# Performance work log

Measured on AMD Instinct MI355X. Metric: run time of the kernel, lower is better.

## Reference

```python
import jax, jax.numpy as jnp
import numpy as np

B, Hh, Ww, C = 32, 56, 56, 256
WIN, SHIFT, HEADS = 7, 3, 8
N = WIN * WIN
nW = (Hh // WIN) * (Ww // WIN)


def _rel_pos_index(w):
    coords = np.stack(np.meshgrid(np.arange(w), np.arange(w), indexing='ij'))  # (2,w,w)
    flat = coords.reshape(2, -1)
    rel = (flat[:, :, None] - flat[:, None, :]).transpose(1, 2, 0)  # (N,N,2)
    rel[..., 0] += w - 1
    rel[..., 1] += w - 1
    rel[..., 0] *= 2 * w - 1
    return rel.sum(-1)  # (N,N) int


def _shift_attn_mask(H, W, w, s):
    img = np.zeros((H, W))
    cnt = 0
    for hs in (slice(0, -w), slice(-w, -s), slice(-s, None)):
        for ws in (slice(0, -w), slice(-w, -s), slice(-s, None)):
            img[hs, ws] = cnt
            cnt += 1
    mw = img.reshape(H // w, w, W // w, w).transpose(0, 2, 1, 3).reshape(-1, w * w)  # (nW,N)
    diff = mw[:, None, :] - mw[:, :, None]
    return np.where(diff != 0, -100.0, 0.0).astype(np.float32)  # (nW,N,N)


REL_IDX = jnp.asarray(_rel_pos_index(WIN))


def layer_norm(x, g, b):
    m = x.mean(-1, keepdims=True)
    v = ((x - m) ** 2).mean(-1, keepdims=True)
    return (x - m) / jnp.sqrt(v + 1e-5) * g + b


def setup_inputs() -> dict:
    key = jax.random.key(0)
    ks = jax.random.split(key, 10)
    s02 = 0.02
    x = jax.random.normal(ks[0], (B, Hh * Ww, C), jnp.float32)
    qkv_w = jax.random.normal(ks[1], (3 * C, C), jnp.float32) * s02
    qkv_b = jnp.zeros((3 * C,), jnp.float32)
    rpb_table = jax.random.normal(ks[2], ((2 * WIN - 1) ** 2, HEADS), jnp.float32) * s02
    proj_w = jax.random.normal(ks[3], (C, C), jnp.float32) * s02
    proj_b = jnp.zeros((C,), jnp.float32)
    fc1_w = jax.random.normal(ks[4], (4 * C, C), jnp.float32) * s02
    fc1_b = jnp.zeros((4 * C,), jnp.float32)
    fc2_w = jax.random.normal(ks[5], (C, 4 * C), jnp.float32) * s02
    fc2_b = jnp.zeros((C,), jnp.float32)
    attn_mask = jnp.asarray(_shift_attn_mask(Hh, Ww, WIN, SHIFT))
    # saliency masks: per-token binary fg/bg -> additive 0/-100 key masks
    fg_tok = jax.random.bernoulli(ks[6], 0.5, (B * nW, N))
    sal_fg = jnp.where(fg_tok[:, None, :], 0.0, -100.0) * jnp.ones((1, N, 1), jnp.float32)
    sal_bg = jnp.where(fg_tok[:, None, :], -100.0, 0.0) * jnp.ones((1, N, 1), jnp.float32)
    return dict(x=x, qkv_w=qkv_w, qkv_b=qkv_b, rpb_table=rpb_table, proj_w=proj_w,
                proj_b=proj_b, norm1_g=jnp.ones((C,)), norm1_b=jnp.zeros((C,)),
                norm2_g=jnp.ones((C,)), norm2_b=jnp.zeros((C,)),
                fc1_w=fc1_w, fc1_b=fc1_b, fc2_w=fc2_w, fc2_b=fc2_b,
                attn_mask=attn_mask, sal_fg_attn_mask=sal_fg.astype(jnp.float32),
                sal_bg_attn_mask=sal_bg.astype(jnp.float32))


def reference(x, qkv_w, qkv_b, rpb_table, proj_w, proj_b, norm1_g, norm1_b,
              norm2_g, norm2_b, fc1_w, fc1_b, fc2_w, fc2_b,
              attn_mask, sal_fg_attn_mask, sal_bg_attn_mask):
    Bb, L, Cc = x.shape
    d = Cc // HEADS
    scale = d ** -0.5
    shortcut = x
    xn = layer_norm(x, norm1_g, norm1_b).reshape(Bb, Hh, Ww, Cc)
    xs = jnp.roll(xn, (-SHIFT, -SHIFT), axis=(1, 2))
    # window partition -> (B*nW, N, C)
    nh = Hh // WIN
    xw = xs.reshape(Bb, nh, WIN, nh, WIN, Cc).transpose(0, 1, 3, 2, 4, 5).reshape(-1, N, Cc)
    B_ = xw.shape[0]
    qkv = (xw @ qkv_w.T + qkv_b).reshape(B_, N, 3, HEADS, d).transpose(2, 0, 3, 1, 4)
    q, k, v = qkv[0] * scale, qkv[1], qkv[2]  # (B_, h, N, d)
    attn = jnp.einsum('bhnd,bhmd->bhnm', q, k)
    rpb = rpb_table[REL_IDX.reshape(-1)].reshape(N, N, HEADS).transpose(2, 0, 1)
    attn = attn + rpb[None]
    attn_fg = attn + sal_fg_attn_mask[:, None]
    attn_bg = attn + sal_bg_attn_mask[:, None]

    def add_shift(a):
        a = a.reshape(B_ // nW, nW, HEADS, N, N) + attn_mask[None, :, None]
        return a.reshape(B_, HEADS, N, N)

    p = jax.nn.softmax(add_shift(attn), axis=-1)
    p_fg = jax.nn.softmax(add_shift(attn_fg), axis=-1)
    p_bg = jax.nn.softmax(add_shift(attn_bg), axis=-1)
    o = jnp.einsum('bhnm,bhmd->bhnd', p + p_fg - p_bg, v)
    o = o.transpose(0, 2, 1, 3).reshape(B_, N, Cc)
    o = o @ proj_w.T + proj_b
    # window reverse + reverse shift
    xr = o.reshape(Bb, nh, nh, WIN, WIN, Cc).transpose(0, 1, 3, 2, 4, 5).reshape(Bb, Hh, Ww, Cc)
    xr = jnp.roll(xr, (SHIFT, SHIFT), axis=(1, 2)).reshape(Bb, L, Cc)
    x = shortcut + xr
    h = layer_norm(x, norm2_g, norm2_b)
    h = jax.nn.gelu(h @ fc1_w.T + fc1_b, approximate=False) @ fc2_w.T + fc2_b
    return x + h
```

## Files before the change

### kernel.cpp

```cpp
#include <hip/hip_runtime.h>
#include <hip/hip_bf16.h>

#define HH 56
#define WWD 56
#define WIN 7
#define SHIFT 3
#define HEADS 8
#define NTOK 49
#define NW 64
#define CDIM 256
#define DH 32
#define MROWS 100352
#define SCALE_Q 0.17677669529663687f

typedef float floatx4 __attribute__((ext_vector_type(4)));
typedef __bf16 bf16x8 __attribute__((ext_vector_type(8)));

__device__ __forceinline__ float wave_sum(float v) {
#pragma unroll
    for (int m = 1; m < 64; m <<= 1) v += __shfl_xor(v, m);
    return v;
}

__device__ __forceinline__ void glds16(const void* g, void* l) {
    __builtin_amdgcn_global_load_lds(
        (const __attribute__((address_space(1))) void*)g,
        (__attribute__((address_space(3))) void*)l, 16, 0, 0);
}

__global__ __launch_bounds__(256) void convert_weights_kernel(
    const float* __restrict__ qkv_w, const float* __restrict__ proj_w,
    const float* __restrict__ fc1_w, const float* __restrict__ fc2_w,
    __hip_bfloat16* __restrict__ dst)
{
    int i = blockIdx.x * 256 + threadIdx.x;
    float v;
    if (i < 196608)       v = qkv_w[i];
    else if (i < 262144)  v = proj_w[i - 196608];
    else if (i < 524288)  v = fc1_w[i - 262144];
    else                  v = fc2_w[i - 524288];
    dst[i] = __float2bfloat16(v);
}

template <bool SHIFTED>
__global__ __launch_bounds__(256) void ln_kernel(
    const float* __restrict__ x, const float* __restrict__ g,
    const float* __restrict__ bb, __hip_bfloat16* __restrict__ out)
{
    const int tok  = blockIdx.x * 4 + (threadIdx.x >> 6);
    const int lane = threadIdx.x & 63;
    const int c    = lane * 4;

    float4 v = *reinterpret_cast<const float4*>(x + (size_t)tok * CDIM + c);
    float s = v.x + v.y + v.z + v.w;
    s = wave_sum(s);
    const float mean = s * (1.0f / 256.0f);
    float d0 = v.x - mean, d1 = v.y - mean, d2 = v.z - mean, d3 = v.w - mean;
    float sq = d0 * d0 + d1 * d1 + d2 * d2 + d3 * d3;
    sq = wave_sum(sq);
    const float rstd = rsqrtf(sq * (1.0f / 256.0f) + 1e-5f);

    float4 gv = *reinterpret_cast<const float4*>(g + c);
    float4 bv = *reinterpret_cast<const float4*>(bb + c);

    union { __hip_bfloat16 h[4]; uint2 u; } pk;
    pk.h[0] = __float2bfloat16(d0 * rstd * gv.x + bv.x);
    pk.h[1] = __float2bfloat16(d1 * rstd * gv.y + bv.y);
    pk.h[2] = __float2bfloat16(d2 * rstd * gv.z + bv.z);
    pk.h[3] = __float2bfloat16(d3 * rstd * gv.w + bv.w);

    size_t oidx;
    if (SHIFTED) {
        int b = tok / 3136;
        int l = tok - b * 3136;
        int h = l / WWD, w = l - (l / WWD) * WWD;
        int hp = h - SHIFT; if (hp < 0) hp += HH;
        int wp = w - SHIFT; if (wp < 0) wp += WWD;
        int bwin = b * NW + (hp / WIN) * 8 + (wp / WIN);
        int n = (hp % WIN) * WIN + (wp % WIN);
        oidx = ((size_t)bwin * NTOK + n) * CDIM + c;
    } else {
        oidx = (size_t)tok * CDIM + c;
    }
    *reinterpret_cast<uint2*>(out + oidx) = pk.u;
}

template <int MODE>
__global__ __launch_bounds__(256) void gemm_kernel(
    const __hip_bfloat16* __restrict__ A,
    const __hip_bfloat16* __restrict__ Wt,
    const float* __restrict__ bias,
    void* __restrict__ outv,
    const float* __restrict__ aux,
    int M, int Nn, int K)
{
    __shared__ __hip_bfloat16 As[128 * 32];
    __shared__ __hip_bfloat16 Bs[128 * 32];

    const int t = threadIdx.x;
    const int wave = t >> 6, lane = t & 63;
    const int m0 = blockIdx.y * 128, n0 = blockIdx.x * 128;
    const int wr = (wave >> 1) * 64;
    const int wc = (wave & 1) * 64;

    floatx4 acc[4][4] = {};

    const int c0 = wave * 64 + lane;
    const int c1 = 256 + c0;
    const int r0 = c0 >> 2, p0 = c0 & 3, g0 = p0 ^ ((r0 >> 1) & 3);
    const int r1 = c1 >> 2, p1 = c1 & 3, g1 = p1 ^ ((r1 >> 1) & 3);
    const __hip_bfloat16* gA0 = A  + (size_t)(m0 + r0) * K + g0 * 8;
    const __hip_bfloat16* gA1 = A  + (size_t)(m0 + r1) * K + g1 * 8;
    const __hip_bfloat16* gB0 = Wt + (size_t)(n0 + r0) * K + g0 * 8;
    const __hip_bfloat16* gB1 = Wt + (size_t)(n0 + r1) * K + g1 * 8;
    const int base0 = (wave * 64) * 8;
    const int base1 = (256 + wave * 64) * 8;

    const int fm = lane & 15;
    const int g4 = lane >> 4;

    for (int k0 = 0; k0 < K; k0 += 32) {
        __syncthreads();
        glds16(gA0 + k0, As + base0);
        glds16(gA1 + k0, As + base1);
        glds16(gB0 + k0, Bs + base0);
        glds16(gB1 + k0, Bs + base1);
        __syncthreads();

        bf16x8 af[4], bfr[4];
#pragma unroll
        for (int mt = 0; mt < 4; ++mt) {
            const int ml = wr + mt * 16 + fm;
            af[mt] = *reinterpret_cast<const bf16x8*>(
                As + ml * 32 + ((g4 ^ ((ml >> 1) & 3)) * 8));
            const int nl = wc + mt * 16 + fm;
            bfr[mt] = *reinterpret_cast<const bf16x8*>(
                Bs + nl * 32 + ((g4 ^ ((nl >> 1) & 3)) * 8));
        }
#pragma unroll
        for (int mt = 0; mt < 4; ++mt)
#pragma unroll
            for (int nt = 0; nt < 4; ++nt)
                acc[mt][nt] = __builtin_amdgcn_mfma_f32_16x16x32_bf16(
                    af[mt], bfr[nt], acc[mt][nt], 0, 0, 0);
    }

    float bv[4];
#pragma unroll
    for (int nt = 0; nt < 4; ++nt) bv[nt] = bias[n0 + wc + nt * 16 + fm];

#pragma unroll
    for (int mt = 0; mt < 4; ++mt) {
#pragma unroll
        for (int r = 0; r < 4; ++r) {
            const int m_g = m0 + wr + mt * 16 + g4 * 4 + r;
            size_t row_idx = 0;
            if (MODE == 1) {
                int bwin = m_g / NTOK;
                int ntok = m_g - bwin * NTOK;
                int b = bwin >> 6, wi = bwin & 63;
                int rr = ntok / WIN, cc = ntok - rr * WIN;
                int hp = (wi >> 3) * WIN + rr;
                int wp = (wi & 7) * WIN + cc;
                int h = hp + SHIFT; if (h >= HH) h -= HH;
                int w = wp + SHIFT; if (w >= WWD) w -= WWD;
                row_idx = ((size_t)b * 3136 + h * WWD + w) * CDIM;
            }
#pragma unroll
            for (int nt = 0; nt < 4; ++nt) {
                const int n_g = n0 + wc + nt * 16 + fm;
                float val = acc[mt][nt][r] + bv[nt];
                if (MODE == 0) {
                    if (n_g < 256) val *= SCALE_Q;
                    reinterpret_cast<__hip_bfloat16*>(outv)[(size_t)m_g * Nn + n_g] =
                        __float2bfloat16(val);
                } else if (MODE == 2) {
                    float gl = 0.5f * val * (1.0f + erff(val * 0.70710678118654752f));
                    reinterpret_cast<__hip_bfloat16*>(outv)[(size_t)m_g * Nn + n_g] =
                        __float2bfloat16(gl);
                } else if (MODE == 3) {
                    size_t idx = (size_t)m_g * CDIM + n_g;
                    reinterpret_cast<float*>(outv)[idx] = aux[idx] + val;
                } else {
                    size_t idx = row_idx + n_g;
                    reinterpret_cast<float*>(outv)[idx] = aux[idx] + val;
                }
            }
        }
    }
}

__global__ __launch_bounds__(256) void attn_kernel(
    const __hip_bfloat16* __restrict__ qkv,
    const float* __restrict__ rpb_table,
    const float* __restrict__ sal_fg,
    __hip_bfloat16* __restrict__ o)
{
    __shared__ unsigned short Pl[4][64 * 40];
    __shared__ unsigned short Vt[4][32 * 72];
    __shared__ float rpb_l[4][176];

    const int t = threadIdx.x;
    const int wave = t >> 6, lane = t & 63;
    const int lane15 = lane & 15, g4 = lane >> 4;
    const int b_ = blockIdx.x >> 1;
    const int h = ((blockIdx.x & 1) << 2) | wave;

    unsigned short* Pw = Pl[wave];
    unsigned short* Vw = Vt[wave];
    float* rpbw = rpb_l[wave];

    const unsigned short* qkv_u = reinterpret_cast<const unsigned short*>(qkv);
    const size_t base = (size_t)b_ * (NTOK * 768) + h * DH;

#pragma unroll
    for (int it = 0; it < 32; ++it) {
        int idx = it * 64 + lane;
        int key = idx >> 5, d = idx & 31;
        unsigned short v = (key < NTOK) ? qkv_u[base + key * 768 + 512 + d]
                                        : (unsigned short)0;
        Vw[d * 72 + key] = v;
    }
#pragma unroll
    for (int it = 0; it < 3; ++it) {
        int i = it * 64 + lane;
        if (i < 169) rpbw[i] = rpb_table[i * 8 + h];
    }
    float sfv = (lane < NTOK) ? sal_fg[(size_t)b_ * (NTOK * NTOK) + lane] : -100.f;
    const unsigned long long fgmask = __ballot(sfv == 0.0f);

    bf16x8 kf[4], qf[4];
#pragma unroll
    for (int mt = 0; mt < 4; ++mt)
        kf[mt] = *reinterpret_cast<const bf16x8*>(
            qkv_u + base + (size_t)(mt * 16 + lane15) * 768 + 256 + g4 * 8);
#pragma unroll
    for (int nt = 0; nt < 4; ++nt)
        qf[nt] = *reinterpret_cast<const bf16x8*>(
            qkv_u + base + (size_t)(nt * 16 + lane15) * 768 + g4 * 8);

    floatx4 S[4][4] = {};
#pragma unroll
    for (int mt = 0; mt < 4; ++mt)
#pragma unroll
        for (int nt = 0; nt < 4; ++nt)
            S[mt][nt] = __builtin_amdgcn_mfma_f32_16x16x32_bf16(
                kf[mt], qf[nt], S[mt][nt], 0, 0, 0);

    const int wr_ = (b_ & 63) >> 3, wc_ = (b_ & 63) & 7;
    int qlin[4], qreg[4];
#pragma unroll
    for (int nt = 0; nt < 4; ++nt) {
        int q = nt * 16 + lane15;
        int qr = (q * 147) >> 10, qc = q - qr * 7;
        qlin[nt] = q + 6 * qr + 84;
        qreg[nt] = ((wr_ == 7) ? ((qr < 4) ? 1 : 2) : 0) * 3
                 + ((wc_ == 7) ? ((qc < 4) ? 1 : 2) : 0);
    }

#pragma unroll
    for (int mt = 0; mt < 4; ++mt)
#pragma unroll
        for (int r = 0; r < 4; ++r) {
            int key = mt * 16 + g4 * 4 + r;
            int kr = (key * 147) >> 10, kc = key - kr * 7;
            int klin = key + 6 * kr;
            int kreg = ((wr_ == 7) ? ((kr < 4) ? 1 : 2) : 0) * 3
                     + ((wc_ == 7) ? ((kc < 4) ? 1 : 2) : 0);
            bool pad = key >= NTOK;
#pragma unroll
            for (int nt = 0; nt < 4; ++nt) {
                int idx = qlin[nt] - klin;
                idx = idx < 0 ? 0 : (idx > 168 ? 168 : idx);
                float s = S[mt][nt][r] + rpbw[idx]
                        + ((qreg[nt] == kreg) ? 0.f : -100.f);
                S[mt][nt][r] = pad ? -1e30f : s;
            }
        }

    float Cfg[4], Cbg[4];
#pragma unroll
    for (int nt = 0; nt < 4; ++nt) {
        float mfg = -3e38f, mbg = -3e38f;
#pragma unroll
        for (int mt = 0; mt < 4; ++mt)
#pragma unroll
            for (int r = 0; r < 4; ++r) {
                int key = mt * 16 + g4 * 4 + r;
                bool fg = (fgmask >> key) & 1ULL;
                float s = S[mt][nt][r];
                mfg = fg ? fmaxf(mfg, s) : mfg;
                mbg = fg ? mbg : fmaxf(mbg, s);
            }
        mfg = fmaxf(mfg, __shfl_xor(mfg, 16)); mfg = fmaxf(mfg, __shfl_xor(mfg, 32));
        mbg = fmaxf(mbg, __shfl_xor(mbg, 16)); mbg = fmaxf(mbg, __shfl_xor(mbg, 32));
        float t1 = 0.f, t2 = 0.f;
#pragma unroll
        for (int mt = 0; mt < 4; ++mt)
#pragma unroll
            for (int r = 0; r < 4; ++r) {
                int key = mt * 16 + g4 * 4 + r;
                bool fg = (fgmask >> key) & 1ULL;
                float e = __expf(S[mt][nt][r] - (fg ? mfg : mbg));
                S[mt][nt][r] = e;
                t1 += fg ? e : 0.f;
                t2 += fg ? 0.f : e;
            }
        t1 += __shfl_xor(t1, 16); t1 += __shfl_xor(t1, 32);
        t2 += __shfl_xor(t2, 16); t2 += __shfl_xor(t2, 32);
        const float m0 = fmaxf(mfg, mbg);
        const float m1 = fmaxf(mfg, mbg - 100.f);
        const float m2 = fmaxf(mfg - 100.f, mbg);
        const float a1 = __expf(mfg - m0),          a2 = __expf(mbg - m0);
        const float b1 = __expf(mfg - m1),          b2 = __expf(mbg - 100.f - m1);
        const float c1 = __expf(mfg - 100.f - m2),  c2 = __expf(mbg - m2);
        const float r0 = 1.f / (t1 * a1 + t2 * a2);
        const float r1 = 1.f / (t1 * b1 + t2 * b2);
        const float r2 = 1.f / (t1 * c1 + t2 * c2);
        Cfg[nt] = a1 * r0 + b1 * r1 - c1 * r2;
        Cbg[nt] = a2 * r0 + b2 * r1 - c2 * r2;
    }

    floatx4 Oc[4][2] = {};
#pragma unroll
    for (int kc = 0; kc < 2; ++kc) {
#pragma unroll
        for (int mh = 0; mh < 2; ++mh) {
            const int mt = kc * 2 + mh;
#pragma unroll
            for (int rp = 0; rp < 2; ++rp) {
                const int key0 = mt * 16 + g4 * 4 + 2 * rp;
                const bool fg0 = (fgmask >> key0) & 1ULL;
                const bool fg1 = (fgmask >> (key0 + 1)) & 1ULL;
                const int keyLocal = key0 - kc * 32;
#pragma unroll
                for (int nt = 0; nt < 4; ++nt) {
                    float pA = S[mt][nt][2 * rp]     * (fg0 ? Cfg[nt] : Cbg[nt]);
                    float pB = S[mt][nt][2 * rp + 1] * (fg1 ? Cfg[nt] : Cbg[nt]);
                    union { __hip_bfloat16 hh[2]; unsigned u; } pk;
                    pk.hh[0] = __float2bfloat16(pA);
                    pk.hh[1] = __float2bfloat16(pB);
                    const int q = nt * 16 + lane15;
                    *reinterpret_cast<unsigned*>(Pw + q * 40 + keyLocal) = pk.u;
                }
            }
        }
        bf16x8 pa[4], vb[2];
#pragma unroll
        for (int mtile = 0; mtile < 4; ++mtile)
            pa[mtile] = *reinterpret_cast<const bf16x8*>(
                Pw + (mtile * 16 + lane15) * 40 + g4 * 8);
#pragma unroll
        for (int n2 = 0; n2 < 2; ++n2)
            vb[n2] = *reinterpret_cast<const bf16x8*>(
                Vw + (n2 * 16 + lane15) * 72 + kc * 32 + g4 * 8);
#pragma unroll
        for (int mtile = 0; mtile < 4; ++mtile)
#pragma unroll
            for (int n2 = 0; n2 < 2; ++n2)
                Oc[mtile][n2] = __builtin_amdgcn_mfma_f32_16x16x32_bf16(
                    pa[mtile], vb[n2], Oc[mtile][n2], 0, 0, 0);
    }

#pragma unroll
    for (int mt = 0; mt < 4; ++mt)
#pragma unroll
        for (int r = 0; r < 4; ++r) {
            int query = mt * 16 + g4 * 4 + r;
            if (query < NTOK) {
                __hip_bfloat16* op = o + ((size_t)b_ * NTOK + query) * CDIM + h * DH;
#pragma unroll
                for (int n2 = 0; n2 < 2; ++n2)
                    op[n2 * 16 + lane15] = __float2bfloat16(Oc[mt][n2][r]);
            }
        }
}

extern "C" void kernel_launch(void* const* d_in, const int* in_sizes, int n_in,
                              void* d_out, int out_size, void* d_ws, size_t ws_size,
                              hipStream_t stream)
{
    const float* x        = (const float*)d_in[0];
    const float* qkv_w    = (const float*)d_in[1];
    const float* qkv_b    = (const float*)d_in[2];
    const float* rpb_tab  = (const float*)d_in[3];
    const float* proj_w   = (const float*)d_in[4];
    const float* proj_b   = (const float*)d_in[5];
    const float* n1g      = (const float*)d_in[6];
    const float* n1b      = (const float*)d_in[7];
    const float* n2g      = (const float*)d_in[8];
    const float* n2b      = (const float*)d_in[9];
    const float* fc1_w    = (const float*)d_in[10];
    const float* fc1_b    = (const float*)d_in[11];
    const float* fc2_w    = (const float*)d_in[12];
    const float* fc2_b    = (const float*)d_in[13];
    const float* sal_fg   = (const float*)d_in[15];

    char* ws = (char*)d_ws;
    __hip_bfloat16* regA = (__hip_bfloat16*)ws;
    __hip_bfloat16* regB = (__hip_bfloat16*)(ws + 205520896);
    float*          x2   = (float*)(ws + 205520896 + 51380224);
    __hip_bfloat16* wbf  = (__hip_bfloat16*)(ws + 205520896 + 51380224 + 102760448);
    __hip_bfloat16* wqkv  = wbf;
    __hip_bfloat16* wproj = wbf + 196608;
    __hip_bfloat16* wfc1  = wbf + 262144;
    __hip_bfloat16* wfc2  = wbf + 524288;

    convert_weights_kernel<<<3072, 256, 0, stream>>>(qkv_w, proj_w, fc1_w, fc2_w, wbf);

    ln_kernel<true><<<MROWS / 4, 256, 0, stream>>>(x, n1g, n1b, regB);

    gemm_kernel<0><<<dim3(768 / 128, MROWS / 128), 256, 0, stream>>>(
        regB, wqkv, qkv_b, regA, nullptr, MROWS, 768, 256);

    attn_kernel<<<2048 * 2, 256, 0, stream>>>(regA, rpb_tab, sal_fg, regB);

    gemm_kernel<1><<<dim3(256 / 128, MROWS / 128), 256, 0, stream>>>(
        regB, wproj, proj_b, x2, x, MROWS, 256, 256);

    ln_kernel<false><<<MROWS / 4, 256, 0, stream>>>(x2, n2g, n2b, regB);

    gemm_kernel<2><<<dim3(1024 / 128, MROWS / 128), 256, 0, stream>>>(
        regB, wfc1, fc1_b, regA, nullptr, MROWS, 1024, 256);

    gemm_kernel<3><<<dim3(256 / 128, MROWS / 128), 256, 0, stream>>>(
        regA, wfc2, fc2_b, d_out, x2, MROWS, 256, 1024);
}
```

Measured before the change: 722.3 us.

## Triple-buffer GEMM LDS loads and remap workgroups across XCDs

Replaces the single-buffered K loop, which needed two barriers per step, with a three-stage LDS ring. Tiles are prefetched two iterations ahead, and explicit vmcnt waits plus one barrier per step let global-to-LDS loads overlap MFMA work. Workgroup IDs are also remapped so that consecutive tiles land on the same XCD, which should improve L2 reuse. LDS use triples, which may reduce occupancy, and correctness relies on the hand-placed waitcnt counts.

New measurement: 705.2 us. 1.02x faster.

```diff
diff --git a/kernel.cpp b/kernel.cpp
--- a/kernel.cpp
+++ b/kernel.cpp
@@ -94,12 +94,21 @@
     const float* __restrict__ aux,
     int M, int Nn, int K)
 {
-    __shared__ __hip_bfloat16 As[128 * 32];
-    __shared__ __hip_bfloat16 Bs[128 * 32];
+    __shared__ __hip_bfloat16 As[3][128 * 32];
+    __shared__ __hip_bfloat16 Bs[3][128 * 32];
 
     const int t = threadIdx.x;
     const int wave = t >> 6, lane = t & 63;
-    const int m0 = blockIdx.y * 128, n0 = blockIdx.x * 128;
+
+    const int nwg  = gridDim.x * gridDim.y;
+    const int orig = blockIdx.y * gridDim.x + blockIdx.x;
+    const int q = nwg >> 3, r = nwg & 7;
+    const int xcd = orig & 7, loc = orig >> 3;
+    const int lin = (xcd < r ? xcd * (q + 1) : r * (q + 1) + (xcd - r) * q) + loc;
+    const int bx = lin % gridDim.x;
+    const int by = lin / gridDim.x;
+
+    const int m0 = by * 128, n0 = bx * 128;
     const int wr = (wave >> 1) * 64;
     const int wc = (wave & 1) * 64;
 
@@ -119,57 +128,86 @@
     const int fm = lane & 15;
     const int g4 = lane >> 4;
 
-    for (int k0 = 0; k0 < K; k0 += 32) {
-        __syncthreads();
-        glds16(gA0 + k0, As + base0);
-        glds16(gA1 + k0, As + base1);
-        glds16(gB0 + k0, Bs + base0);
-        glds16(gB1 + k0, Bs + base1);
-        __syncthreads();
-
+    const int nt = K >> 5;
+
+    glds16(gA0,      As[0] + base0);
+    glds16(gA1,      As[0] + base1);
+    glds16(gB0,      Bs[0] + base0);
+    glds16(gB1,      Bs[0] + base1);
+    glds16(gA0 + 32, As[1] + base0);
+    glds16(gA1 + 32, As[1] + base1);
+    glds16(gB0 + 32, Bs[1] + base0);
+    glds16(gB1 + 32, Bs[1] + base1);
+    asm volatile("s_waitcnt vmcnt(4)" ::: "memory");
+    __builtin_amdgcn_s_barrier();
+    __builtin_amdgcn_sched_barrier(0);
+
+    int cur = 0;
+    for (int tt = 0; tt < nt; ++tt) {
+        if (tt + 2 < nt) {
+            const int nx2 = (cur >= 1) ? cur - 1 : cur + 2;
+            const int k2 = (tt + 2) << 5;
+            glds16(gA0 + k2, As[nx2] + base0);
+            glds16(gA1 + k2, As[nx2] + base1);
+            glds16(gB0 + k2, Bs[nx2] + base0);
+            glds16(gB1 + k2, Bs[nx2] + base1);
+        }
+
+        const __hip_bfloat16* Ac = As[cur];
+        const __hip_bfloat16* Bc = Bs[cur];
         bf16x8 af[4], bfr[4];
 #pragma unroll
         for (int mt = 0; mt < 4; ++mt) {
             const int ml = wr + mt * 16 + fm;
             af[mt] = *reinterpret_cast<const bf16x8*>(
-                As + ml * 32 + ((g4 ^ ((ml >> 1) & 3)) * 8));
+                Ac + ml * 32 + ((g4 ^ ((ml >> 1) & 3)) * 8));
             const int nl = wc + mt * 16 + fm;
             bfr[mt] = *reinterpret_cast<const bf16x8*>(
-                Bs + nl * 32 + ((g4 ^ ((nl >> 1) & 3)) * 8));
+                Bc + nl * 32 + ((g4 ^ ((nl >> 1) & 3)) * 8));
         }
 #pragma unroll
         for (int mt = 0; mt < 4; ++mt)
 #pragma unroll
-            for (int nt = 0; nt < 4; ++nt)
-                acc[mt][nt] = __builtin_amdgcn_mfma_f32_16x16x32_bf16(
-                    af[mt], bfr[nt], acc[mt][nt], 0, 0, 0);
+            for (int nn = 0; nn < 4; ++nn)
+                acc[mt][nn] = __builtin_amdgcn_mfma_f32_16x16x32_bf16(
+                    af[mt], bfr[nn], acc[mt][nn], 0, 0, 0);
+
+        if (tt + 1 < nt) {
+            if (tt + 2 < nt)
+                asm volatile("s_waitcnt vmcnt(4) lgkmcnt(0)" ::: "memory");
+            else
+                asm volatile("s_waitcnt vmcnt(0) lgkmcnt(0)" ::: "memory");
+            __builtin_amdgcn_s_barrier();
+            __builtin_amdgcn_sched_barrier(0);
+        }
+        cur = (cur >= 2) ? 0 : cur + 1;
     }
 
     float bv[4];
 #pragma unroll
-    for (int nt = 0; nt < 4; ++nt) bv[nt] = bias[n0 + wc + nt * 16 + fm];
+    for (int nn = 0; nn < 4; ++nn) bv[nn] = bias[n0 + wc + nn * 16 + fm];
 
 #pragma unroll
     for (int mt = 0; mt < 4; ++mt) {
 #pragma unroll
-        for (int r = 0; r < 4; ++r) {
-            const int m_g = m0 + wr + mt * 16 + g4 * 4 + r;
+        for (int rr = 0; rr < 4; ++rr) {
+            const int m_g = m0 + wr + mt * 16 + g4 * 4 + rr;
             size_t row_idx = 0;
             if (MODE == 1) {
                 int bwin = m_g / NTOK;
                 int ntok = m_g - bwin * NTOK;
                 int b = bwin >> 6, wi = bwin & 63;
-                int rr = ntok / WIN, cc = ntok - rr * WIN;
-                int hp = (wi >> 3) * WIN + rr;
+                int r2 = ntok / WIN, cc = ntok - r2 * WIN;
+                int hp = (wi >> 3) * WIN + r2;
                 int wp = (wi & 7) * WIN + cc;
                 int h = hp + SHIFT; if (h >= HH) h -= HH;
                 int w = wp + SHIFT; if (w >= WWD) w -= WWD;
                 row_idx = ((size_t)b * 3136 + h * WWD + w) * CDIM;
             }
 #pragma unroll
-            for (int nt = 0; nt < 4; ++nt) {
-                const int n_g = n0 + wc + nt * 16 + fm;
-                float val = acc[mt][nt][r] + bv[nt];
+            for (int nn = 0; nn < 4; ++nn) {
+                const int n_g = n0 + wc + nn * 16 + fm;
+                float val = acc[mt][nn][rr] + bv[nn];
                 if (MODE == 0) {
                     if (n_g < 256) val *= SCALE_Q;
                     reinterpret_cast<__hip_bfloat16*>(outv)[(size_t)m_g * Nn + n_g] =
```
